# Optimization experiments

Hardware: AMD Instinct MI355X
Metric: run time of the kernel (lower is better)

The kernel has to match this reference:

```python
import jax, jax.numpy as jnp
import numpy as np

HIDDEN = 1024
HEADS = 16
HEAD_DIM = HIDDEN // HEADS
B, L = 4, 2048


def setup_inputs() -> dict:
    key = jax.random.key(0)
    ks = jax.random.split(key, 9)
    s = 1.0 / np.sqrt(HIDDEN)
    inp = {
        "x": jax.random.normal(ks[0], (B, L, HIDDEN), dtype=jnp.float32),
        "wq": jax.random.uniform(ks[1], (HIDDEN, HIDDEN), jnp.float32, -s, s),
        "bq": jax.random.uniform(ks[2], (HIDDEN,), jnp.float32, -s, s),
        "wk": jax.random.uniform(ks[3], (HIDDEN, HIDDEN), jnp.float32, -s, s),
        "bk": jax.random.uniform(ks[4], (HIDDEN,), jnp.float32, -s, s),
        "wv": jax.random.uniform(ks[5], (HIDDEN, HIDDEN), jnp.float32, -s, s),
        "bv": jax.random.uniform(ks[6], (HIDDEN,), jnp.float32, -s, s),
        "wo": jax.random.uniform(ks[7], (HIDDEN, HIDDEN), jnp.float32, -s, s),
        "bo": jax.random.uniform(ks[8], (HIDDEN,), jnp.float32, -s, s),
    }
    return inp


def reference(x, wq, bq, wk, bk, wv, bv, wo, bo):
    b, l, d = x.shape
    # projections (torch Linear: x @ W^T + b; here weights stored as [in,out])
    q = x @ wq + bq
    k = x @ wk + bk
    v = x @ wv + bv
    # [b, h, l, hd]
    q = q.reshape(b, l, HEADS, HEAD_DIM).transpose(0, 2, 1, 3)
    k = k.reshape(b, l, HEADS, HEAD_DIM).transpose(0, 2, 1, 3)
    v = v.reshape(b, l, HEADS, HEAD_DIM).transpose(0, 2, 1, 3)
    scale = 1.0 / np.sqrt(HEAD_DIM).astype(np.float32)
    score = jnp.einsum('bhqd,bhkd->bhqk', q, k) * scale
    attn = jax.nn.softmax(score, axis=-1)
    out = jnp.einsum('bhqk,bhkd->bhqd', attn, v)
    out = out.transpose(0, 2, 1, 3).reshape(b, l, d)
    return out @ wo + bo
```

## Files before the change

kernel.cpp:

```cpp
#include <hip/hip_runtime.h>
#include <hip/hip_bf16.h>
#include <cstdint>

#define HIDDEN 1024
#define HEADS 16
#define HEAD_DIM 64
#define BATCH 4
#define SEQ 2048
#define TOK (BATCH * SEQ)

typedef __attribute__((ext_vector_type(8))) short short8;
typedef __attribute__((ext_vector_type(4))) float f32x4;
typedef __attribute__((ext_vector_type(16))) float f32x16;

__device__ __forceinline__ void gload_lds16(const void* g, void* s) {
  __builtin_amdgcn_global_load_lds(
      (const __attribute__((address_space(1))) void*)g,
      (__attribute__((address_space(3))) void*)s, 16, 0, 0);
}

__device__ __forceinline__ unsigned short f2bf(float x) {
  union { __hip_bfloat16 h; unsigned short u; } c;
  c.h = __float2bfloat16(x);
  return c.u;
}

__device__ __forceinline__ uint32_t cvt_pk_bf16(float lo, float hi) {
  uint32_t r;
  asm("v_cvt_pk_bf16_f32 %0, %1, %2" : "=v"(r) : "v"(lo), "v"(hi));
  return r;
}

__global__ __launch_bounds__(256) void convert_f32_bf16(
    const float* __restrict__ in, __hip_bfloat16* __restrict__ out, int n4) {
  int idx = blockIdx.x * blockDim.x + threadIdx.x;
  int stride = gridDim.x * blockDim.x;
  for (int i = idx; i < n4; i += stride) {
    float4 v = ((const float4*)in)[i];
    union { ushort4 u; __hip_bfloat16 h[4]; } r;
    r.h[0] = __float2bfloat16(v.x);
    r.h[1] = __float2bfloat16(v.y);
    r.h[2] = __float2bfloat16(v.z);
    r.h[3] = __float2bfloat16(v.w);
    ((ushort4*)out)[i] = r.u;
  }
}

__global__ __launch_bounds__(256) void transpose_to_bf16(
    const float* __restrict__ in, __hip_bfloat16* __restrict__ out) {
  __shared__ __hip_bfloat16 t[64][65];
  const int tx = threadIdx.x & 63;
  const int ty = threadIdx.x >> 6;
  const int k0 = blockIdx.y * 64;
  const int n0 = blockIdx.x * 64;
#pragma unroll
  for (int i = 0; i < 16; ++i) {
    int r = i * 4 + ty;
    t[r][tx] = __float2bfloat16(in[(size_t)(k0 + r) * 1024 + n0 + tx]);
  }
  __syncthreads();
#pragma unroll
  for (int i = 0; i < 16; ++i) {
    int r = i * 4 + ty;
    out[(size_t)(n0 + r) * 1024 + k0 + tx] = t[tx][r];
  }
}

template <int EPI, int KDIM>
__global__ __launch_bounds__(256) void gemm128(
    const __hip_bfloat16* __restrict__ A, const __hip_bfloat16* __restrict__ Bt,
    float* __restrict__ Cout, const float* __restrict__ bias,
    const float* __restrict__ bq, const float* __restrict__ bk,
    const float* __restrict__ bv, __hip_bfloat16* __restrict__ Qb,
    __hip_bfloat16* __restrict__ Kb, __hip_bfloat16* __restrict__ VTb) {
  __shared__ __hip_bfloat16 As[128 * 32];
  __shared__ __hip_bfloat16 Bs[128 * 32];
  const int tid = threadIdx.x;
  const int w = tid >> 6, l = tid & 63;
  const int lc = l & 15, lg = l >> 4;
  const int wr = w >> 1, wc = w & 1;
  const int bm0 = blockIdx.x * 128;
  const int bn0 = blockIdx.y * 128;
  const int lrow = l >> 2;
  const int lk = (l & 3) * 8;

  f32x4 acc[4][4] = {};

#pragma unroll 1
  for (int kt = 0; kt < KDIM; kt += 32) {
    if (w < 2) {
#pragma unroll
      for (int i = 0; i < 4; ++i) {
        int rloc = w * 64 + i * 16;
        const __hip_bfloat16* src =
            A + (size_t)(bm0 + rloc + lrow) * KDIM + kt + lk;
        gload_lds16(src, &As[rloc * 32]);
      }
    } else {
#pragma unroll
      for (int i = 0; i < 4; ++i) {
        int rloc = (w - 2) * 64 + i * 16;
        const __hip_bfloat16* src =
            Bt + (size_t)(bn0 + rloc + lrow) * KDIM + kt + lk;
        gload_lds16(src, &Bs[rloc * 32]);
      }
    }
    __syncthreads();
    short8 af[4], bf[4];
#pragma unroll
    for (int mt = 0; mt < 4; ++mt)
      af[mt] = *(const short8*)&As[(wr * 64 + mt * 16 + lc) * 32 + 8 * lg];
#pragma unroll
    for (int nt = 0; nt < 4; ++nt)
      bf[nt] = *(const short8*)&Bs[(wc * 64 + nt * 16 + lc) * 32 + 8 * lg];
#pragma unroll
    for (int mt = 0; mt < 4; ++mt)
#pragma unroll
      for (int nt = 0; nt < 4; ++nt)
        acc[mt][nt] = __builtin_amdgcn_mfma_f32_16x16x32_bf16(
            af[mt], bf[nt], acc[mt][nt], 0, 0, 0);
    __syncthreads();
  }

#pragma unroll
  for (int mt = 0; mt < 4; ++mt) {
#pragma unroll
    for (int nt = 0; nt < 4; ++nt) {
#pragma unroll
      for (int r = 0; r < 4; ++r) {
        int m = bm0 + wr * 64 + mt * 16 + 4 * lg + r;
        int n = bn0 + wc * 64 + nt * 16 + lc;
        float v = acc[mt][nt][r];
        if (EPI == 0) {
          Cout[(size_t)m * 1024 + n] = v + bias[n];
        } else {
          int proj = n >> 10, win = n & 1023, h = win >> 6, d = win & 63;
          const float* bp = (proj == 0) ? bq : ((proj == 1) ? bk : bv);
          __hip_bfloat16 hv = __float2bfloat16(v + bp[win]);
          int b = m >> 11, lq = m & 2047;
          if (proj == 0)
            Qb[((size_t)(b * 16 + h) * 2048 + lq) * 64 + d] = hv;
          else if (proj == 1)
            Kb[((size_t)(b * 16 + h) * 2048 + lq) * 64 + d] = hv;
          else
            VTb[((size_t)(b * 16 + h) * 64 + d) * 2048 + lq] = hv;
        }
      }
    }
  }
}

__global__ __launch_bounds__(256, 4) void attn32(
    const __hip_bfloat16* __restrict__ Qb, const __hip_bfloat16* __restrict__ Kb,
    const __hip_bfloat16* __restrict__ VTb, __hip_bfloat16* __restrict__ AO) {
  __shared__ __align__(16) char lds[2][2][8192];
  const int tid = threadIdx.x;
  const int w = tid >> 6, l = tid & 63;
  const int q32 = l & 31;
  const int hi = l >> 5;
  const int bh = blockIdx.y;
  const int qb = blockIdx.x;
  const int b = bh >> 4, h = bh & 15;

  const __hip_bfloat16* Qp = Qb + (size_t)bh * SEQ * 64;
  const char* Kg = (const char*)(Kb + (size_t)bh * SEQ * 64);
  const char* Vg = (const char*)(VTb + (size_t)bh * 64 * SEQ);

  const int q0w = qb * 128 + w * 32;
  short8 qf[4];
#pragma unroll
  for (int ds = 0; ds < 4; ++ds)
    qf[ds] = *(const short8*)(Qp + (size_t)(q0w + q32) * 64 + ds * 16 + 8 * hi);

  const int srow = l >> 3;
  const int scol = (16 * (l & 7)) ^ (srow << 4);
  const int i0 = 2 * w, i1 = 2 * w + 1;

#define STAGE_KV(buf, kv0)                                                   \
  {                                                                          \
    gload_lds16(Kg + (size_t)((kv0) + i0 * 8 + srow) * 128 + scol,           \
                &lds[buf][0][i0 * 1024]);                                    \
    gload_lds16(Kg + (size_t)((kv0) + i1 * 8 + srow) * 128 + scol,           \
                &lds[buf][0][i1 * 1024]);                                    \
    gload_lds16(Vg + (size_t)(i0 * 8 + srow) * (SEQ * 2) +                   \
                    (size_t)(kv0) * 2 + scol,                                \
                &lds[buf][1][i0 * 1024]);                                    \
    gload_lds16(Vg + (size_t)(i1 * 8 + srow) * (SEQ * 2) +                   \
                    (size_t)(kv0) * 2 + scol,                                \
                &lds[buf][1][i1 * 1024]);                                    \
  }

  STAGE_KV(0, 0);

  f32x16 o0 = {}, o1 = {};
  float mrun = -INFINITY, lrun = 0.0f;
  const float cs = 0.125f * 1.44269504088896f;
  const int swz = (q32 & 7) << 4;

#pragma unroll 1
  for (int it = 0; it < 32; ++it) {
    const int kv0 = it * 64;
    const int cur = it & 1;
    __syncthreads();
    if (it < 31) STAGE_KV(cur ^ 1, kv0 + 64);

    const char* Kt = lds[cur][0];
    f32x16 s0 = {}, s1 = {};
#pragma unroll
    for (int ds = 0; ds < 4; ++ds) {
      const int c = (32 * ds + 16 * hi) ^ swz;
      short8 k0 = *(const short8*)(Kt + q32 * 128 + c);
      short8 k1 = *(const short8*)(Kt + (32 + q32) * 128 + c);
      s0 = __builtin_amdgcn_mfma_f32_32x32x16_bf16(k0, qf[ds], s0, 0, 0, 0);
      s1 = __builtin_amdgcn_mfma_f32_32x32x16_bf16(k1, qf[ds], s1, 0, 0, 0);
    }

#define M3F(a, b, c) fmaxf(fmaxf((a), (b)), (c))
    float u0 = M3F(s0[0], s0[1], s0[2]);
    float u1 = M3F(s0[3], s0[4], s0[5]);
    float u2 = M3F(s0[6], s0[7], s0[8]);
    float u3 = M3F(s0[9], s0[10], s0[11]);
    float u4 = M3F(s0[12], s0[13], s0[14]);
    float u5 = M3F(s0[15], s1[0], s1[1]);
    float u6 = M3F(s1[2], s1[3], s1[4]);
    float u7 = M3F(s1[5], s1[6], s1[7]);
    float u8 = M3F(s1[8], s1[9], s1[10]);
    float u9 = M3F(s1[11], s1[12], s1[13]);
    float ua = fmaxf(s1[14], s1[15]);
    float t =
        M3F(M3F(u0, u1, u2), M3F(u3, u4, u5), M3F(M3F(u6, u7, u8), u9, ua));
#undef M3F
    t = fmaxf(t, __shfl_xor(t, 32));
    const float tl = t * cs;

    const bool nores = (__all(tl <= mrun + 8.0f) != 0);
    const float mn = nores ? mrun : fmaxf(mrun, tl);

    float p0[16], p1[16];
    float rs = 0.0f;
#pragma unroll
    for (int i = 0; i < 16; ++i) {
      p0[i] = exp2f(fmaf(s0[i], cs, -mn));
      p1[i] = exp2f(fmaf(s1[i], cs, -mn));
      rs += p0[i] + p1[i];
    }
    rs += __shfl_xor(rs, 32);

    if (!nores) {
      const float corr = exp2f(mrun - mn);
      mrun = mn;
      lrun *= corr;
      o0 *= corr;
      o1 *= corr;
    }
    lrun += rs;

    uint32_t pw[4][4];
#pragma unroll
    for (int ks = 0; ks < 4; ++ks) {
      const int base = 8 * (ks & 1);
#pragma unroll
      for (int g = 0; g < 4; ++g) {
        float lo = (ks < 2) ? p0[base + 2 * g] : p1[base + 2 * g];
        float hp = (ks < 2) ? p0[base + 2 * g + 1] : p1[base + 2 * g + 1];
        pw[ks][g] = cvt_pk_bf16(lo, hp);
      }
    }

    const char* Vt = lds[cur][1];
#pragma unroll
    for (int ks = 0; ks < 4; ++ks) {
      union { short8 v; uint32_t u[4]; } pb;
      pb.u[0] = pw[ks][0];
      pb.u[1] = pw[ks][1];
      pb.u[2] = pw[ks][2];
      pb.u[3] = pw[ks][3];
      const int cA = (32 * ks + 8 * hi) ^ swz;
      const int cB = (32 * ks + 16 + 8 * hi) ^ swz;
      union { short8 v; uint64_t u[2]; } a0, a1;
      a0.u[0] = *(const uint64_t*)(Vt + q32 * 128 + cA);
      a0.u[1] = *(const uint64_t*)(Vt + q32 * 128 + cB);
      a1.u[0] = *(const uint64_t*)(Vt + (32 + q32) * 128 + cA);
      a1.u[1] = *(const uint64_t*)(Vt + (32 + q32) * 128 + cB);
      o0 = __builtin_amdgcn_mfma_f32_32x32x16_bf16(a0.v, pb.v, o0, 0, 0, 0);
      o1 = __builtin_amdgcn_mfma_f32_32x32x16_bf16(a1.v, pb.v, o1, 0, 0, 0);
    }
  }

  const float rinv = 1.0f / lrun;
  const size_t orow = (size_t)(b * SEQ + q0w + q32) * 1024 + h * 64;
#pragma unroll
  for (int g = 0; g < 4; ++g) {
    uint2 wa, wb;
    wa.x = cvt_pk_bf16(o0[4 * g + 0] * rinv, o0[4 * g + 1] * rinv);
    wa.y = cvt_pk_bf16(o0[4 * g + 2] * rinv, o0[4 * g + 3] * rinv);
    wb.x = cvt_pk_bf16(o1[4 * g + 0] * rinv, o1[4 * g + 1] * rinv);
    wb.y = cvt_pk_bf16(o1[4 * g + 2] * rinv, o1[4 * g + 3] * rinv);
    *(uint2*)(AO + orow + 8 * g + 4 * hi) = wa;
    *(uint2*)(AO + orow + 32 + 8 * g + 4 * hi) = wb;
  }
#undef STAGE_KV
}

extern "C" void kernel_launch(void* const* d_in, const int* in_sizes, int n_in,
                              void* d_out, int out_size, void* d_ws,
                              size_t ws_size, hipStream_t stream) {
  const float* x = (const float*)d_in[0];
  const float* wq = (const float*)d_in[1];
  const float* bq = (const float*)d_in[2];
  const float* wk = (const float*)d_in[3];
  const float* bk = (const float*)d_in[4];
  const float* wv = (const float*)d_in[5];
  const float* bv = (const float*)d_in[6];
  const float* wo = (const float*)d_in[7];
  const float* bo = (const float*)d_in[8];
  float* out = (float*)d_out;
  char* ws = (char*)d_ws;

  __hip_bfloat16* XB = (__hip_bfloat16*)(ws);
  __hip_bfloat16* WT = (__hip_bfloat16*)(ws + (16ull << 20));
  __hip_bfloat16* WOT = (__hip_bfloat16*)(ws + (22ull << 20));
  __hip_bfloat16* QB = (__hip_bfloat16*)(ws + (24ull << 20));
  __hip_bfloat16* KB = (__hip_bfloat16*)(ws + (40ull << 20));
  __hip_bfloat16* VTB = (__hip_bfloat16*)(ws + (56ull << 20));
  __hip_bfloat16* AO = XB;

  convert_f32_bf16<<<2048, 256, 0, stream>>>(x, XB, TOK * HIDDEN / 4);
  transpose_to_bf16<<<dim3(16, 16), 256, 0, stream>>>(wq, WT);
  transpose_to_bf16<<<dim3(16, 16), 256, 0, stream>>>(wk, WT + 1024 * 1024);
  transpose_to_bf16<<<dim3(16, 16), 256, 0, stream>>>(wv, WT + 2 * 1024 * 1024);
  transpose_to_bf16<<<dim3(16, 16), 256, 0, stream>>>(wo, WOT);

  gemm128<1, 1024><<<dim3(64, 24), 256, 0, stream>>>(
      XB, WT, nullptr, nullptr, bq, bk, bv, QB, KB, VTB);

  attn32<<<dim3(16, 64), 256, 0, stream>>>(QB, KB, VTB, AO);

  gemm128<0, 1024><<<dim3(64, 8), 256, 0, stream>>>(
      AO, WOT, out, bo, nullptr, nullptr, nullptr, nullptr, nullptr, nullptr);
}
```

Measured before the change: 349.4 us.

## Replace QKV projection GEMM with 256x256-tile 8-wave pipelined kernel

```diff
diff --git a/kernel.cpp b/kernel.cpp
--- a/kernel.cpp
+++ b/kernel.cpp
@@ -29,6 +29,10 @@
   uint32_t r;
   asm("v_cvt_pk_bf16_f32 %0, %1, %2" : "=v"(r) : "v"(lo), "v"(hi));
   return r;
+}
+
+__device__ __forceinline__ f32x4 mfma16(short8 a, short8 b, f32x4 c) {
+  return __builtin_amdgcn_mfma_f32_16x16x32_bf16(a, b, c, 0, 0, 0);
 }
 
 __global__ __launch_bounds__(256) void convert_f32_bf16(
@@ -63,6 +67,168 @@
   for (int i = 0; i < 16; ++i) {
     int r = i * 4 + ty;
     out[(size_t)(n0 + r) * 1024 + k0 + tx] = t[tx][r];
+  }
+}
+
+__global__ __launch_bounds__(512, 2) void gemm256_qkv(
+    const __hip_bfloat16* __restrict__ A, const __hip_bfloat16* __restrict__ Bt,
+    const float* __restrict__ bq, const float* __restrict__ bk,
+    const float* __restrict__ bv, __hip_bfloat16* __restrict__ Qb,
+    __hip_bfloat16* __restrict__ Kb, __hip_bfloat16* __restrict__ VTb) {
+  __shared__ __align__(16) char lds[2][4][16384];
+  const int tid = threadIdx.x;
+  const int wv = tid >> 6, l = tid & 63;
+  const int lc = l & 15, lg4 = l >> 4;
+
+  const int nwg = gridDim.x, cpx = nwg >> 3;
+  const int bid = (blockIdx.x & 7) * cpx + (blockIdx.x >> 3);
+  const int tm = bid / 12, tn = bid % 12;
+  const int bm0 = tm * 256, bn0 = tn * 256;
+
+  const int wm = wv >> 2, wn = wv & 3;
+
+  const int r0 = 8 * wv + (l >> 3);
+  const int scol = (16 * (l & 7)) ^ ((l & 32) ? 32 : 0);
+  const char* Ab = (const char*)A;
+  const char* Bb = (const char*)Bt;
+
+#define ST1(buf, reg, gB, rowb, kt, c)                                        \
+  gload_lds16(gB + (size_t)((rowb) + 64 * (c) + r0) * 2048 +                  \
+                  (size_t)(kt) * 128 + scol,                                  \
+              &lds[buf][reg][(c) * 8192 + wv * 1024])
+#define STAGE_KT(buf, kt)                                                     \
+  {                                                                           \
+    ST1(buf, 0, Ab, bm0, kt, 0);                                              \
+    ST1(buf, 0, Ab, bm0, kt, 1);                                              \
+    ST1(buf, 1, Ab, bm0 + 128, kt, 0);                                        \
+    ST1(buf, 1, Ab, bm0 + 128, kt, 1);                                        \
+    ST1(buf, 2, Bb, bn0, kt, 0);                                              \
+    ST1(buf, 2, Bb, bn0, kt, 1);                                              \
+    ST1(buf, 3, Bb, bn0 + 128, kt, 0);                                        \
+    ST1(buf, 3, Bb, bn0 + 128, kt, 1);                                        \
+  }
+
+  const int alg = (16 * lg4) ^ ((lc & 4) << 3);
+  const int brow0 = (64 * (wn & 1)) * 128;
+
+  short8 af[4][2];
+  short8 b0[2][2];
+  short8 b1[2][2];
+  f32x4 acc[8][4] = {};
+
+  STAGE_KT(0, 0);
+  STAGE_KT(1, 1);
+  asm volatile("s_waitcnt vmcnt(8)" ::: "memory");
+  __builtin_amdgcn_s_barrier();
+
+#pragma unroll 1
+  for (int kt = 0; kt < 16; ++kt) {
+    const int cur = kt & 1;
+    const char* Ar = &lds[cur][wm][0];
+    const char* Br = &lds[cur][2 + (wn >> 1)][0];
+
+#pragma unroll
+    for (int mf = 0; mf < 4; ++mf)
+#pragma unroll
+      for (int ks = 0; ks < 2; ++ks)
+        af[mf][ks] =
+            *(const short8*)(Ar + (16 * mf + lc) * 128 + 64 * ks + alg);
+#pragma unroll
+    for (int nf = 0; nf < 2; ++nf)
+#pragma unroll
+      for (int ks = 0; ks < 2; ++ks)
+        b0[nf][ks] = *(const short8*)(Br + brow0 + (16 * nf + lc) * 128 +
+                                      64 * ks + alg);
+    __builtin_amdgcn_s_barrier();
+    __builtin_amdgcn_s_setprio(1);
+#pragma unroll
+    for (int mf = 0; mf < 4; ++mf)
+#pragma unroll
+      for (int nf = 0; nf < 2; ++nf) {
+        acc[mf][nf] = mfma16(af[mf][0], b0[nf][0], acc[mf][nf]);
+        acc[mf][nf] = mfma16(af[mf][1], b0[nf][1], acc[mf][nf]);
+      }
+    __builtin_amdgcn_s_setprio(0);
+    __builtin_amdgcn_s_barrier();
+
+#pragma unroll
+    for (int nf = 0; nf < 2; ++nf)
+#pragma unroll
+      for (int ks = 0; ks < 2; ++ks)
+        b1[nf][ks] = *(const short8*)(Br + brow0 + (32 + 16 * nf + lc) * 128 +
+                                      64 * ks + alg);
+    __builtin_amdgcn_s_barrier();
+    __builtin_amdgcn_s_setprio(1);
+#pragma unroll
+    for (int mf = 0; mf < 4; ++mf)
+#pragma unroll
+      for (int nf = 0; nf < 2; ++nf) {
+        acc[mf][2 + nf] = mfma16(af[mf][0], b1[nf][0], acc[mf][2 + nf]);
+        acc[mf][2 + nf] = mfma16(af[mf][1], b1[nf][1], acc[mf][2 + nf]);
+      }
+    __builtin_amdgcn_s_setprio(0);
+    __builtin_amdgcn_s_barrier();
+
+#pragma unroll
+    for (int mf = 0; mf < 4; ++mf)
+#pragma unroll
+      for (int ks = 0; ks < 2; ++ks)
+        af[mf][ks] =
+            *(const short8*)(Ar + (64 + 16 * mf + lc) * 128 + 64 * ks + alg);
+    __builtin_amdgcn_s_barrier();
+    __builtin_amdgcn_s_setprio(1);
+#pragma unroll
+    for (int mf = 0; mf < 4; ++mf)
+#pragma unroll
+      for (int nf = 0; nf < 2; ++nf) {
+        acc[4 + mf][2 + nf] = mfma16(af[mf][0], b1[nf][0], acc[4 + mf][2 + nf]);
+        acc[4 + mf][2 + nf] = mfma16(af[mf][1], b1[nf][1], acc[4 + mf][2 + nf]);
+      }
+    __builtin_amdgcn_s_setprio(0);
+    __builtin_amdgcn_s_barrier();
+
+    if (kt < 14) {
+      STAGE_KT(cur, kt + 2);
+      asm volatile("s_waitcnt vmcnt(8)" ::: "memory");
+    } else {
+      asm volatile("s_waitcnt vmcnt(0)" ::: "memory");
+    }
+    __builtin_amdgcn_s_barrier();
+    __builtin_amdgcn_s_setprio(1);
+#pragma unroll
+    for (int mf = 0; mf < 4; ++mf)
+#pragma unroll
+      for (int nf = 0; nf < 2; ++nf) {
+        acc[4 + mf][nf] = mfma16(af[mf][0], b0[nf][0], acc[4 + mf][nf]);
+        acc[4 + mf][nf] = mfma16(af[mf][1], b0[nf][1], acc[4 + mf][nf]);
+      }
+    __builtin_amdgcn_s_setprio(0);
+    __builtin_amdgcn_s_barrier();
+  }
+#undef STAGE_KT
+#undef ST1
+
+#pragma unroll
+  for (int mf = 0; mf < 8; ++mf) {
+#pragma unroll
+    for (int nf = 0; nf < 4; ++nf) {
+#pragma unroll
+      for (int r = 0; r < 4; ++r) {
+        int m = bm0 + 128 * wm + 16 * mf + 4 * lg4 + r;
+        int n = bn0 + 64 * wn + 16 * nf + lc;
+        float v = acc[mf][nf][r];
+        int proj = n >> 10, win = n & 1023, h = win >> 6, d = win & 63;
+        const float* bp = (proj == 0) ? bq : ((proj == 1) ? bk : bv);
+        __hip_bfloat16 hv = __float2bfloat16(v + bp[win]);
+        int b = m >> 11, lq = m & 2047;
+        if (proj == 0)
+          Qb[((size_t)(b * 16 + h) * 2048 + lq) * 64 + d] = hv;
+        else if (proj == 1)
+          Kb[((size_t)(b * 16 + h) * 2048 + lq) * 64 + d] = hv;
+        else
+          VTb[((size_t)(b * 16 + h) * 64 + d) * 2048 + lq] = hv;
+      }
+    }
   }
 }
 
@@ -331,8 +497,7 @@
   transpose_to_bf16<<<dim3(16, 16), 256, 0, stream>>>(wv, WT + 2 * 1024 * 1024);
   transpose_to_bf16<<<dim3(16, 16), 256, 0, stream>>>(wo, WOT);
 
-  gemm128<1, 1024><<<dim3(64, 24), 256, 0, stream>>>(
-      XB, WT, nullptr, nullptr, bq, bk, bv, QB, KB, VTB);
+  gemm256_qkv<<<384, 512, 0, stream>>>(XB, WT, bq, bk, bv, QB, KB, VTB);
 
   attn32<<<dim3(16, 64), 256, 0, stream>>>(QB, KB, VTB, AO);
 
```

New measurement: 362.3 us. +3.7%, slower.
